# Kernel tuning notes

Measured on AMD Instinct MI355X. Metric: run time of the kernel, lower is better.

Reference implementation:

```python
import jax, jax.numpy as jnp
import numpy as np
import math

SEQ, BATCH, H, E, V = 2048, 64, 512, 256, 50257


def _gru_cell(x, h, W_ih, W_hh, b_ih, b_hh):
    # PyTorch GRU cell: gates ordered (r, z, n)
    gi = x @ W_ih.T + b_ih            # [B, 3H]
    gh = h @ W_hh.T + b_hh            # [B, 3H]
    i_r, i_z, i_n = jnp.split(gi, 3, axis=1)
    h_r, h_z, h_n = jnp.split(gh, 3, axis=1)
    r = jax.nn.sigmoid(i_r + h_r)
    z = jax.nn.sigmoid(i_z + h_z)
    n = jnp.tanh(i_n + r * h_n)
    return (1.0 - z) * n + z * h


def setup_inputs() -> dict:
    key = jax.random.key(0)
    ks = jax.random.split(key, 14)
    s = 1.0 / math.sqrt(H)
    inp = {
        "inputs": jax.random.randint(ks[0], (BATCH,), 0, V),
        "dec_hidden": jax.random.normal(ks[1], (2, BATCH, H), jnp.float32),
        "enc_outputs": jax.random.normal(ks[2], (SEQ, BATCH, H), jnp.float32),
        "emb": jax.random.normal(ks[3], (V, E), jnp.float32),
        # layer 0: input dim = H + E
        "W_ih0": jax.random.uniform(ks[4], (3 * H, H + E), jnp.float32, -s, s),
        "W_hh0": jax.random.uniform(ks[5], (3 * H, H), jnp.float32, -s, s),
        "b_ih0": jax.random.uniform(ks[6], (3 * H,), jnp.float32, -s, s),
        "b_hh0": jax.random.uniform(ks[7], (3 * H,), jnp.float32, -s, s),
        # layer 1: input dim = H
        "W_ih1": jax.random.uniform(ks[8], (3 * H, H), jnp.float32, -s, s),
        "W_hh1": jax.random.uniform(ks[9], (3 * H, H), jnp.float32, -s, s),
        "b_ih1": jax.random.uniform(ks[10], (3 * H,), jnp.float32, -s, s),
        "b_hh1": jax.random.uniform(ks[11], (3 * H,), jnp.float32, -s, s),
        "out_W": jax.random.uniform(ks[12], (V, H), jnp.float32, -s, s),
        "out_b": jax.random.uniform(ks[13], (V,), jnp.float32, -s, s),
    }
    return inp


def reference(inputs, dec_hidden, enc_outputs, emb,
              W_ih0, W_hh0, b_ih0, b_hh0,
              W_ih1, W_hh1, b_ih1, b_hh1,
              out_W, out_b):
    # --- dot-product attention (vectorized over seq) ---
    h_top = dec_hidden[-1]                                     # [B, H]
    scale = 1.0 / math.sqrt(H)
    energy = jnp.einsum('bh,sbh->sb', h_top, enc_outputs) * scale  # [S, B]
    alpha = jax.nn.softmax(energy, axis=0)                     # softmax over seq
    context = jnp.einsum('sb,sbh->bh', alpha, enc_outputs)     # [B, H]
    # --- embed + concat ---
    embeddings = emb[inputs]                                   # [B, E]
    x = jnp.concatenate([embeddings, context], axis=1)         # [B, E+H]
    # --- 2-layer GRU, single time step (eval mode: no dropout) ---
    h0 = _gru_cell(x, dec_hidden[0], W_ih0, W_hh0, b_ih0, b_hh0)
    h1 = _gru_cell(h0, dec_hidden[1], W_ih1, W_hh1, b_ih1, b_hh1)
    new_hidden = jnp.stack([h0, h1], axis=0)                   # [2, B, H]
    # --- vocab projection ---
    logits = h1 @ out_W.T + out_b                              # [B, V]
    return logits, new_hidden
```

## Files before the change

### kernel.cpp

```cpp
#include <hip/hip_runtime.h>
#include <math.h>

#define SEQ   2048
#define BATCH 64
#define HDIM  512
#define EDIM  256
#define VOCAB 50257
#define BH    (BATCH * HDIM)
#define G3    (3 * HDIM)
#define NCOL  (2 * G3)
#define P32   32
#define KS    4

typedef __attribute__((ext_vector_type(4))) float f32x4;
typedef __attribute__((ext_vector_type(8))) short bf16x8;

__device__ __forceinline__ unsigned short f2bf(float x) {
    unsigned int u = __float_as_uint(x);
    u += 0x7fffu + ((u >> 16) & 1u);
    return (unsigned short)(u >> 16);
}

__device__ __forceinline__ bf16x8 pack8(float4 a, float4 b) {
    bf16x8 r;
    r[0] = (short)f2bf(a.x); r[1] = (short)f2bf(a.y);
    r[2] = (short)f2bf(a.z); r[3] = (short)f2bf(a.w);
    r[4] = (short)f2bf(b.x); r[5] = (short)f2bf(b.y);
    r[6] = (short)f2bf(b.z); r[7] = (short)f2bf(b.w);
    return r;
}

__device__ __forceinline__ bf16x8 cvt8(const float* p) {
    return pack8(*(const float4*)p, *(const float4*)(p + 4));
}

__global__ __launch_bounds__(256)
void attn_partial(const float* __restrict__ enc, const float* __restrict__ dec,
                  float* __restrict__ pm, float* __restrict__ pl,
                  float* __restrict__ pacc) {
    const int lane = threadIdx.x & 63;
    const int w = threadIdx.x >> 6;
    const int p = blockIdx.x;
    const int b = blockIdx.y;
    const int s0 = (p * 4 + w) * 16;
    const float scale = 0.044194173824159216f;

    const float4* qp = (const float4*)(dec + BH + (size_t)b * HDIM + 8 * lane);
    float4 q0 = qp[0], q1 = qp[1];
    float qa[8] = {q0.x, q0.y, q0.z, q0.w, q1.x, q1.y, q1.z, q1.w};

    float m = -INFINITY, l = 0.f;
    float acc[8] = {0.f, 0.f, 0.f, 0.f, 0.f, 0.f, 0.f, 0.f};

    #pragma unroll 2
    for (int r = 0; r < 16; r += 4) {
        float va[4][8];
        #pragma unroll
        for (int j = 0; j < 4; ++j) {
            const float4* vp = (const float4*)(enc +
                ((size_t)(s0 + r + j) * BATCH + b) * HDIM + 8 * lane);
            float4 t0 = vp[0], t1 = vp[1];
            va[j][0] = t0.x; va[j][1] = t0.y; va[j][2] = t0.z; va[j][3] = t0.w;
            va[j][4] = t1.x; va[j][5] = t1.y; va[j][6] = t1.z; va[j][7] = t1.w;
        }
        float e[4];
        #pragma unroll
        for (int j = 0; j < 4; ++j) {
            float d = 0.f;
            #pragma unroll
            for (int i = 0; i < 8; ++i) d = fmaf(va[j][i], qa[i], d);
            e[j] = d;
        }
        #pragma unroll
        for (int off = 32; off > 0; off >>= 1) {
            #pragma unroll
            for (int j = 0; j < 4; ++j) e[j] += __shfl_xor(e[j], off, 64);
        }
        #pragma unroll
        for (int j = 0; j < 4; ++j) e[j] *= scale;
        float m4 = fmaxf(fmaxf(e[0], e[1]), fmaxf(e[2], e[3]));
        float em = fmaxf(m, m4);
        float f  = __expf(m - em);
        float w0 = __expf(e[0] - em), w1 = __expf(e[1] - em);
        float w2 = __expf(e[2] - em), w3 = __expf(e[3] - em);
        l = l * f + (w0 + w1 + w2 + w3);
        #pragma unroll
        for (int i = 0; i < 8; ++i) {
            float a = acc[i] * f;
            a = fmaf(w0, va[0][i], a);
            a = fmaf(w1, va[1][i], a);
            a = fmaf(w2, va[2][i], a);
            acc[i] = fmaf(w3, va[3][i], a);
        }
        m = em;
    }

    __shared__ float sacc[4][HDIM];
    __shared__ float sml[8];
    #pragma unroll
    for (int i = 0; i < 8; ++i) sacc[w][8 * lane + i] = acc[i];
    if (lane == 0) { sml[w] = m; sml[4 + w] = l; }
    __syncthreads();

    const float m0 = sml[0], m1 = sml[1], m2 = sml[2], m3 = sml[3];
    const float ms = fmaxf(fmaxf(m0, m1), fmaxf(m2, m3));
    const float c0 = __expf(m0 - ms), c1 = __expf(m1 - ms);
    const float c2 = __expf(m2 - ms), c3 = __expf(m3 - ms);
    const int t = threadIdx.x;
    #pragma unroll
    for (int i = 0; i < 2; ++i) {
        const int h = t + i * 256;
        float v = c0 * sacc[0][h] + c1 * sacc[1][h]
                + c2 * sacc[2][h] + c3 * sacc[3][h];
        pacc[((size_t)b * P32 + p) * HDIM + h] = v;
    }
    if (t == 0) {
        pm[b * P32 + p] = ms;
        pl[b * P32 + p] = c0 * sml[4] + c1 * sml[5] + c2 * sml[6] + c3 * sml[7];
    }
}

__global__ __launch_bounds__(512)
void attn_combine(const float* __restrict__ pm, const float* __restrict__ pl,
                  const float* __restrict__ pacc, const float* __restrict__ dec,
                  const float* __restrict__ emb, const int* __restrict__ inputs,
                  unsigned short* __restrict__ xbf,
                  unsigned short* __restrict__ d0bf,
                  unsigned short* __restrict__ d1bf) {
    __shared__ float s_coef[P32];
    __shared__ float s_inv;
    const int b = blockIdx.x;
    const int t = threadIdx.x;

    if (t < 64) {
        float mloc = -INFINITY;
        for (int p = t; p < P32; p += 64) mloc = fmaxf(mloc, pm[b * P32 + p]);
        #pragma unroll
        for (int off = 32; off > 0; off >>= 1) mloc = fmaxf(mloc, __shfl_xor(mloc, off, 64));
        float d = 0.f;
        for (int p = t; p < P32; p += 64) {
            float c = __expf(pm[b * P32 + p] - mloc);
            s_coef[p] = c;
            d = fmaf(c, pl[b * P32 + p], d);
        }
        #pragma unroll
        for (int off = 32; off > 0; off >>= 1) d += __shfl_xor(d, off, 64);
        if (t == 0) s_inv = 1.f / d;
    }
    __syncthreads();

    float c = 0.f;
    const float* pa = pacc + (size_t)b * P32 * HDIM + t;
    #pragma unroll 8
    for (int p = 0; p < P32; ++p) c = fmaf(s_coef[p], pa[(size_t)p * HDIM], c);
    float ctx = c * s_inv;

    xbf[(size_t)b * (EDIM + HDIM) + EDIM + t] = f2bf(ctx);
    if (t < EDIM)
        xbf[(size_t)b * (EDIM + HDIM) + t] = f2bf(emb[(size_t)inputs[b] * EDIM + t]);
    d0bf[(size_t)b * HDIM + t] = f2bf(dec[(size_t)b * HDIM + t]);
    d1bf[(size_t)b * HDIM + t] = f2bf(dec[BH + (size_t)b * HDIM + t]);
}

template<int K1>
__global__ __launch_bounds__(256)
void gru_gemm(const unsigned short* __restrict__ Aih,
              const unsigned short* __restrict__ Ahh,
              const float* __restrict__ Wih,
              const float* __restrict__ Whh,
              float* __restrict__ part) {
    const int lane = threadIdx.x & 63;
    const int nt = blockIdx.x * 4 + (threadIdx.x >> 6);
    const int kc = blockIdx.y;
    const int nn = lane & 15;
    const int koff = (lane >> 4) * 8;

    const bool ih = nt < 96;
    const int col16 = ih ? nt : nt - 96;
    const int g = col16 * 16 + nn;
    const int K = ih ? K1 : HDIM;
    const int kchunk = K >> 2;
    const int k0 = kc * kchunk;

    const float* wrow = (ih ? Wih : Whh) + (size_t)g * K + k0 + koff;
    const unsigned short* arow = (ih ? Aih : Ahh) + (size_t)nn * K + k0 + koff;

    f32x4 acc[4];
    #pragma unroll
    for (int mt = 0; mt < 4; ++mt) acc[mt] = (f32x4){0, 0, 0, 0};

    const int nks = kchunk >> 5;
    #pragma unroll 2
    for (int ks = 0; ks < nks; ++ks) {
        bf16x8 bf = cvt8(wrow + 32 * ks);
        #pragma unroll
        for (int mt = 0; mt < 4; ++mt) {
            bf16x8 a = *(const bf16x8*)(arow + (size_t)mt * 16 * K + 32 * ks);
            acc[mt] = __builtin_amdgcn_mfma_f32_16x16x32_bf16(a, bf, acc[mt], 0, 0, 0);
        }
    }

    const int col = col16 * 16 + nn + (ih ? 0 : G3);
    float* pp = part + ((size_t)kc * NCOL + col) * 64 + (lane >> 4) * 4;
    #pragma unroll
    for (int mt = 0; mt < 4; ++mt)
        *(f32x4*)(pp + mt * 16) = acc[mt];
}

__global__ __launch_bounds__(256)
void gru_gate(const float* __restrict__ part,
              const float* __restrict__ hprev,
              const float* __restrict__ bih, const float* __restrict__ bhh,
              float* __restrict__ hout, unsigned short* __restrict__ houtBf) {
    const int gidx = blockIdx.x * 256 + threadIdx.x;
    const int b = gidx & 63;
    const int h = gidx >> 6;

    #define PRD(c) (part[(size_t)(c) * 64 + b] \
                  + part[((size_t)NCOL + (c)) * 64 + b] \
                  + part[((size_t)2 * NCOL + (c)) * 64 + b] \
                  + part[((size_t)3 * NCOL + (c)) * 64 + b])
    float ir = PRD(h),             hr = PRD(G3 + h);
    float iz = PRD(HDIM + h),      hz = PRD(G3 + HDIM + h);
    float in_ = PRD(2 * HDIM + h), hn = PRD(G3 + 2 * HDIM + h);
    #undef PRD

    float r = 1.f / (1.f + __expf(-(ir + bih[h] + hr + bhh[h])));
    float z = 1.f / (1.f + __expf(-(iz + bih[HDIM + h] + hz + bhh[HDIM + h])));
    float n = tanhf(in_ + bih[2 * HDIM + h] + r * (hn + bhh[2 * HDIM + h]));
    float hp = hprev[(size_t)b * HDIM + h];
    float hnew = (1.f - z) * n + z * hp;

    hout[(size_t)b * HDIM + h] = hnew;
    houtBf[(size_t)b * HDIM + h] = f2bf(hnew);
}

__global__ __launch_bounds__(256)
void vocab_proj_mfma(const unsigned short* __restrict__ h1bf,
                     const float* __restrict__ Wout,
                     const float* __restrict__ bout,
                     float* __restrict__ logits) {
    __shared__ uint4 sh4[4096];
    const int t = threadIdx.x;
    const uint4* g4 = (const uint4*)h1bf;
    #pragma unroll
    for (int i = 0; i < 16; ++i) {
        int q = i * 256 + t;
        int r = q >> 6, s = q & 63;
        sh4[(r << 6) | (s ^ (r & 15))] = g4[q];
    }
    __syncthreads();

    const int NT = (VOCAB + 15) / 16;
    const int lane = t & 63;
    const int nt = blockIdx.x * 4 + (t >> 6);
    if (nt >= NT) return;

    const int nn = lane & 15;
    const int koff16 = lane >> 4;
    const int v  = nt * 16 + nn;
    const int vclamp = min(v, VOCAB - 1);

    const float* wrow = Wout + (size_t)vclamp * HDIM + koff16 * 8;

    f32x4 acc[4];
    #pragma unroll
    for (int mt = 0; mt < 4; ++mt) acc[mt] = (f32x4){0, 0, 0, 0};

    float4 pw0[3], pw1[3];
    #pragma unroll
    for (int d = 0; d < 3; ++d) {
        pw0[d] = *(const float4*)(wrow + 32 * d);
        pw1[d] = *(const float4*)(wrow + 32 * d + 4);
    }

    #pragma unroll
    for (int ks = 0; ks < 16; ++ks) {
        const int slot = ks % 3;
        bf16x8 bfrag = pack8(pw0[slot], pw1[slot]);
        if (ks + 3 < 16) {
            pw0[slot] = *(const float4*)(wrow + 32 * (ks + 3));
            pw1[slot] = *(const float4*)(wrow + 32 * (ks + 3) + 4);
        }
        const int s = 4 * ks + koff16;
        #pragma unroll
        for (int mt = 0; mt < 4; ++mt) {
            const int row = mt * 16 + nn;
            bf16x8 a = *(const bf16x8*)&sh4[(row << 6) | (s ^ nn)];
            acc[mt] = __builtin_amdgcn_mfma_f32_16x16x32_bf16(a, bfrag, acc[mt], 0, 0, 0);
        }
    }

    if (v < VOCAB) {
        const float bias = bout[v];
        const int b0 = koff16 * 4;
        #pragma unroll
        for (int mt = 0; mt < 4; ++mt)
            #pragma unroll
            for (int r = 0; r < 4; ++r)
                logits[(size_t)(mt * 16 + b0 + r) * VOCAB + v] = acc[mt][r] + bias;
    }
}

extern "C" void kernel_launch(void* const* d_in, const int* in_sizes, int n_in,
                              void* d_out, int out_size, void* d_ws, size_t ws_size,
                              hipStream_t stream) {
    const int*   inputs = (const int*)d_in[0];
    const float* dec    = (const float*)d_in[1];
    const float* enc    = (const float*)d_in[2];
    const float* emb    = (const float*)d_in[3];
    const float* Wih0   = (const float*)d_in[4];
    const float* Whh0   = (const float*)d_in[5];
    const float* bih0   = (const float*)d_in[6];
    const float* bhh0   = (const float*)d_in[7];
    const float* Wih1   = (const float*)d_in[8];
    const float* Whh1   = (const float*)d_in[9];
    const float* bih1   = (const float*)d_in[10];
    const float* bhh1   = (const float*)d_in[11];
    const float* Wout   = (const float*)d_in[12];
    const float* bout   = (const float*)d_in[13];
    float* out = (float*)d_out;

    float* w    = (float*)d_ws;
    float* pm   = w;
    float* pl   = pm + (size_t)P32 * BATCH;
    float* pacc = pl + (size_t)P32 * BATCH;
    float* part = pacc + (size_t)P32 * BATCH * HDIM;
    unsigned short* xbf  = (unsigned short*)(part + (size_t)KS * NCOL * 64);
    unsigned short* d0bf = xbf + (size_t)BATCH * (EDIM + HDIM);
    unsigned short* d1bf = d0bf + BH;
    unsigned short* h0bf = d1bf + BH;
    unsigned short* h1bf = h0bf + BH;

    float* h0out = out + (size_t)BATCH * VOCAB;
    float* h1out = h0out + BH;

    attn_partial<<<dim3(P32, BATCH), 256, 0, stream>>>(enc, dec, pm, pl, pacc);
    attn_combine<<<BATCH, 512, 0, stream>>>(pm, pl, pacc, dec, emb, inputs, xbf, d0bf, d1bf);

    gru_gemm<EDIM + HDIM><<<dim3(48, KS), 256, 0, stream>>>(xbf, d0bf, Wih0, Whh0, part);
    gru_gate<<<128, 256, 0, stream>>>(part, dec, bih0, bhh0, h0out, h0bf);
    gru_gemm<HDIM><<<dim3(48, KS), 256, 0, stream>>>(h0bf, d1bf, Wih1, Whh1, part);
    gru_gate<<<128, 256, 0, stream>>>(part, dec + BH, bih1, bhh1, h1out, h1bf);

    const int NT = (VOCAB + 15) / 16;
    vocab_proj_mfma<<<(NT + 3) / 4, 256, 0, stream>>>(h1bf, Wout, bout, out);
}
```

Measured before the change: 119.0 us.

## Fuse attention combine and both GRU layers into one persistent kernel with grid barriers

Replaces five separate launches (attention combine, two GRU GEMMs, two gate kernels) with a single 192-block kernel whose phases are separated by atomic-counter grid barriers. The aim is to remove per-launch overhead and inter-kernel gaps on this small, latency-bound middle section. In exchange it adds a memset of the barrier counters, spin-wait barriers whose correctness depends on all 192 blocks being co-resident, and a combine step in which every thread redundantly recomputes the softmax max and coefficients.

```diff
diff --git a/kernel.cpp b/kernel.cpp
--- a/kernel.cpp
+++ b/kernel.cpp
@@ -11,6 +11,7 @@
 #define NCOL  (2 * G3)
 #define P32   32
 #define KS    4
+#define NBLK_MID 192
 
 typedef __attribute__((ext_vector_type(4))) float f32x4;
 typedef __attribute__((ext_vector_type(8))) short bf16x8;
@@ -32,6 +33,16 @@
 
 __device__ __forceinline__ bf16x8 cvt8(const float* p) {
     return pack8(*(const float4*)p, *(const float4*)(p + 4));
+}
+
+__device__ __forceinline__ void gbar(unsigned* cnt, unsigned nb) {
+    __syncthreads();
+    if (threadIdx.x == 0) {
+        __hip_atomic_fetch_add(cnt, 1u, __ATOMIC_ACQ_REL, __HIP_MEMORY_SCOPE_AGENT);
+        while (__hip_atomic_load(cnt, __ATOMIC_ACQUIRE, __HIP_MEMORY_SCOPE_AGENT) < nb)
+            __builtin_amdgcn_s_sleep(2);
+    }
+    __syncthreads();
 }
 
 __global__ __launch_bounds__(256)
@@ -120,58 +131,15 @@
     }
 }
 
-__global__ __launch_bounds__(512)
-void attn_combine(const float* __restrict__ pm, const float* __restrict__ pl,
-                  const float* __restrict__ pacc, const float* __restrict__ dec,
-                  const float* __restrict__ emb, const int* __restrict__ inputs,
-                  unsigned short* __restrict__ xbf,
-                  unsigned short* __restrict__ d0bf,
-                  unsigned short* __restrict__ d1bf) {
-    __shared__ float s_coef[P32];
-    __shared__ float s_inv;
-    const int b = blockIdx.x;
-    const int t = threadIdx.x;
-
-    if (t < 64) {
-        float mloc = -INFINITY;
-        for (int p = t; p < P32; p += 64) mloc = fmaxf(mloc, pm[b * P32 + p]);
-        #pragma unroll
-        for (int off = 32; off > 0; off >>= 1) mloc = fmaxf(mloc, __shfl_xor(mloc, off, 64));
-        float d = 0.f;
-        for (int p = t; p < P32; p += 64) {
-            float c = __expf(pm[b * P32 + p] - mloc);
-            s_coef[p] = c;
-            d = fmaf(c, pl[b * P32 + p], d);
-        }
-        #pragma unroll
-        for (int off = 32; off > 0; off >>= 1) d += __shfl_xor(d, off, 64);
-        if (t == 0) s_inv = 1.f / d;
-    }
-    __syncthreads();
-
-    float c = 0.f;
-    const float* pa = pacc + (size_t)b * P32 * HDIM + t;
-    #pragma unroll 8
-    for (int p = 0; p < P32; ++p) c = fmaf(s_coef[p], pa[(size_t)p * HDIM], c);
-    float ctx = c * s_inv;
-
-    xbf[(size_t)b * (EDIM + HDIM) + EDIM + t] = f2bf(ctx);
-    if (t < EDIM)
-        xbf[(size_t)b * (EDIM + HDIM) + t] = f2bf(emb[(size_t)inputs[b] * EDIM + t]);
-    d0bf[(size_t)b * HDIM + t] = f2bf(dec[(size_t)b * HDIM + t]);
-    d1bf[(size_t)b * HDIM + t] = f2bf(dec[BH + (size_t)b * HDIM + t]);
-}
-
 template<int K1>
-__global__ __launch_bounds__(256)
-void gru_gemm(const unsigned short* __restrict__ Aih,
-              const unsigned short* __restrict__ Ahh,
-              const float* __restrict__ Wih,
-              const float* __restrict__ Whh,
-              float* __restrict__ part) {
-    const int lane = threadIdx.x & 63;
-    const int nt = blockIdx.x * 4 + (threadIdx.x >> 6);
-    const int kc = blockIdx.y;
+__device__ __forceinline__ void gemm_phase(int blk, int tid,
+        const unsigned short* __restrict__ Aih,
+        const unsigned short* __restrict__ Ahh,
+        const float* __restrict__ Wih, const float* __restrict__ Whh,
+        float* __restrict__ part) {
+    const int lane = tid & 63;
+    const int nt = (blk % 48) * 4 + (tid >> 6);
+    const int kc = blk / 48;
     const int nn = lane & 15;
     const int koff = (lane >> 4) * 8;
 
@@ -207,15 +175,12 @@
         *(f32x4*)(pp + mt * 16) = acc[mt];
 }
 
-__global__ __launch_bounds__(256)
-void gru_gate(const float* __restrict__ part,
-              const float* __restrict__ hprev,
-              const float* __restrict__ bih, const float* __restrict__ bhh,
-              float* __restrict__ hout, unsigned short* __restrict__ houtBf) {
-    const int gidx = blockIdx.x * 256 + threadIdx.x;
-    const int b = gidx & 63;
-    const int h = gidx >> 6;
-
+__device__ __forceinline__ void gate_phase(int idx,
+        const float* __restrict__ part, const float* __restrict__ hprev,
+        const float* __restrict__ bih, const float* __restrict__ bhh,
+        float* __restrict__ hout, unsigned short* __restrict__ houtBf) {
+    const int b = idx & 63;
+    const int h = idx >> 6;
     #define PRD(c) (part[(size_t)(c) * 64 + b] \
                   + part[((size_t)NCOL + (c)) * 64 + b] \
                   + part[((size_t)2 * NCOL + (c)) * 64 + b] \
@@ -224,15 +189,66 @@
     float iz = PRD(HDIM + h),      hz = PRD(G3 + HDIM + h);
     float in_ = PRD(2 * HDIM + h), hn = PRD(G3 + 2 * HDIM + h);
     #undef PRD
-
     float r = 1.f / (1.f + __expf(-(ir + bih[h] + hr + bhh[h])));
     float z = 1.f / (1.f + __expf(-(iz + bih[HDIM + h] + hz + bhh[HDIM + h])));
     float n = tanhf(in_ + bih[2 * HDIM + h] + r * (hn + bhh[2 * HDIM + h]));
     float hp = hprev[(size_t)b * HDIM + h];
     float hnew = (1.f - z) * n + z * hp;
-
     hout[(size_t)b * HDIM + h] = hnew;
     houtBf[(size_t)b * HDIM + h] = f2bf(hnew);
+}
+
+__global__ __launch_bounds__(256)
+void mid_fused(unsigned* __restrict__ bars,
+               const float* __restrict__ pm, const float* __restrict__ pl,
+               const float* __restrict__ pacc, const float* __restrict__ dec,
+               const float* __restrict__ emb, const int* __restrict__ inputs,
+               const float* __restrict__ Wih0, const float* __restrict__ Whh0,
+               const float* __restrict__ bih0, const float* __restrict__ bhh0,
+               const float* __restrict__ Wih1, const float* __restrict__ Whh1,
+               const float* __restrict__ bih1, const float* __restrict__ bhh1,
+               unsigned short* __restrict__ xbf, unsigned short* __restrict__ d0bf,
+               unsigned short* __restrict__ d1bf, float* __restrict__ part,
+               float* __restrict__ h0out, unsigned short* __restrict__ h0bf,
+               float* __restrict__ h1out, unsigned short* __restrict__ h1bf) {
+    const int blk = blockIdx.x;
+    const int tid = threadIdx.x;
+    const int idx = blk * 256 + tid;
+
+    if (idx < BH) {
+        const int b = idx >> 9, h = idx & 511;
+        float mmax = -INFINITY;
+        #pragma unroll 8
+        for (int p = 0; p < P32; ++p) mmax = fmaxf(mmax, pm[b * P32 + p]);
+        float denom = 0.f, ctx = 0.f;
+        const float* pa = pacc + (size_t)b * P32 * HDIM + h;
+        #pragma unroll 4
+        for (int p = 0; p < P32; ++p) {
+            float c = __expf(pm[b * P32 + p] - mmax);
+            denom = fmaf(c, pl[b * P32 + p], denom);
+            ctx = fmaf(c, pa[(size_t)p * HDIM], ctx);
+        }
+        ctx *= (1.f / denom);
+        xbf[(size_t)b * (EDIM + HDIM) + EDIM + h] = f2bf(ctx);
+        d0bf[idx] = f2bf(dec[idx]);
+        d1bf[idx] = f2bf(dec[BH + idx]);
+    } else {
+        const int j = idx - BH;
+        const int b = j >> 8, e = j & 255;
+        xbf[(size_t)b * (EDIM + HDIM) + e] = f2bf(emb[(size_t)inputs[b] * EDIM + e]);
+    }
+    gbar(bars + 0, NBLK_MID);
+
+    gemm_phase<EDIM + HDIM>(blk, tid, xbf, d0bf, Wih0, Whh0, part);
+    gbar(bars + 1, NBLK_MID);
+
+    if (idx < BH) gate_phase(idx, part, dec, bih0, bhh0, h0out, h0bf);
+    gbar(bars + 2, NBLK_MID);
+
+    gemm_phase<HDIM>(blk, tid, h0bf, d1bf, Wih1, Whh1, part);
+    gbar(bars + 3, NBLK_MID);
+
+    if (idx < BH) gate_phase(idx, part, dec + BH, bih1, bhh1, h1out, h1bf);
 }
 
 __global__ __launch_bounds__(256)
@@ -321,7 +337,8 @@
     const float* bout   = (const float*)d_in[13];
     float* out = (float*)d_out;
 
-    float* w    = (float*)d_ws;
+    unsigned* bars = (unsigned*)d_ws;
+    float* w    = (float*)((char*)d_ws + 64);
     float* pm   = w;
     float* pl   = pm + (size_t)P32 * BATCH;
     float* pacc = pl + (size_t)P32 * BATCH;
@@ -335,13 +352,15 @@
     float* h0out = out + (size_t)BATCH * VOCAB;
     float* h1out = h0out + BH;
 
+    hipMemsetAsync(bars, 0, 64, stream);
+
     attn_partial<<<dim3(P32, BATCH), 256, 0, stream>>>(enc, dec, pm, pl, pacc);
-    attn_combine<<<BATCH, 512, 0, stream>>>(pm, pl, pacc, dec, emb, inputs, xbf, d0bf, d1bf);
-
-    gru_gemm<EDIM + HDIM><<<dim3(48, KS), 256, 0, stream>>>(xbf, d0bf, Wih0, Whh0, part);
-    gru_gate<<<128, 256, 0, stream>>>(part, dec, bih0, bhh0, h0out, h0bf);
-    gru_gemm<HDIM><<<dim3(48, KS), 256, 0, stream>>>(h0bf, d1bf, Wih1, Whh1, part);
-    gru_gate<<<128, 256, 0, stream>>>(part, dec + BH, bih1, bhh1, h1out, h1bf);
+
+    mid_fused<<<NBLK_MID, 256, 0, stream>>>(bars, pm, pl, pacc, dec, emb, inputs,
+                                            Wih0, Whh0, bih0, bhh0,
+                                            Wih1, Whh1, bih1, bhh1,
+                                            xbf, d0bf, d1bf, part,
+                                            h0out, h0bf, h1out, h1bf);
 
     const int NT = (VOCAB + 15) / 16;
     vocab_proj_mfma<<<(NT + 3) / 4, 256, 0, stream>>>(h1bf, Wout, bout, out);
```

Result: slower. 179.4 us (+50.7%).

## Fuse attention combine into partial kernel via last-block atomic ticket

Applied to the files above, without the earlier changes.

Removes the separate attn_combine launch: each attention partial block increments a per-batch atomic ticket, and the last of the 32 blocks for that batch row merges the partial softmax states and writes the bf16 context, embedding and hidden copies. Encoder loads also switch to nontemporal loads so the streamed data does not pollute the cache. This saves one kernel launch and its gap, at the cost of a serialized tail block per batch row. The ticket is never reset but relies on modulo 32 across calls, and the pacc reads in the last block depend on acquire/release ordering being sufficient.

```diff
diff --git a/kernel.cpp b/kernel.cpp
--- a/kernel.cpp
+++ b/kernel.cpp
@@ -36,8 +36,19 @@
 
 __global__ __launch_bounds__(256)
 void attn_partial(const float* __restrict__ enc, const float* __restrict__ dec,
+                  const float* __restrict__ emb, const int* __restrict__ inputs,
+                  unsigned* __restrict__ ticket,
                   float* __restrict__ pm, float* __restrict__ pl,
-                  float* __restrict__ pacc) {
+                  float* __restrict__ pacc,
+                  unsigned short* __restrict__ xbf,
+                  unsigned short* __restrict__ d0bf,
+                  unsigned short* __restrict__ d1bf) {
+    __shared__ float sacc[4][HDIM];
+    __shared__ float sml[8];
+    __shared__ unsigned s_old;
+    __shared__ float cs[P32];
+    __shared__ float s_inv;
+
     const int lane = threadIdx.x & 63;
     const int w = threadIdx.x >> 6;
     const int p = blockIdx.x;
@@ -57,11 +68,12 @@
         float va[4][8];
         #pragma unroll
         for (int j = 0; j < 4; ++j) {
-            const float4* vp = (const float4*)(enc +
+            const f32x4* vp = (const f32x4*)(enc +
                 ((size_t)(s0 + r + j) * BATCH + b) * HDIM + 8 * lane);
-            float4 t0 = vp[0], t1 = vp[1];
-            va[j][0] = t0.x; va[j][1] = t0.y; va[j][2] = t0.z; va[j][3] = t0.w;
-            va[j][4] = t1.x; va[j][5] = t1.y; va[j][6] = t1.z; va[j][7] = t1.w;
+            f32x4 t0 = __builtin_nontemporal_load(vp);
+            f32x4 t1 = __builtin_nontemporal_load(vp + 1);
+            #pragma unroll
+            for (int i = 0; i < 4; ++i) { va[j][i] = t0[i]; va[j][4 + i] = t1[i]; }
         }
         float e[4];
         #pragma unroll
@@ -95,8 +107,6 @@
         m = em;
     }
 
-    __shared__ float sacc[4][HDIM];
-    __shared__ float sml[8];
     #pragma unroll
     for (int i = 0; i < 8; ++i) sacc[w][8 * lane + i] = acc[i];
     if (lane == 0) { sml[w] = m; sml[4 + w] = l; }
@@ -118,48 +128,42 @@
         pm[b * P32 + p] = ms;
         pl[b * P32 + p] = c0 * sml[4] + c1 * sml[5] + c2 * sml[6] + c3 * sml[7];
     }
-}
-
-__global__ __launch_bounds__(512)
-void attn_combine(const float* __restrict__ pm, const float* __restrict__ pl,
-                  const float* __restrict__ pacc, const float* __restrict__ dec,
-                  const float* __restrict__ emb, const int* __restrict__ inputs,
-                  unsigned short* __restrict__ xbf,
-                  unsigned short* __restrict__ d0bf,
-                  unsigned short* __restrict__ d1bf) {
-    __shared__ float s_coef[P32];
-    __shared__ float s_inv;
-    const int b = blockIdx.x;
-    const int t = threadIdx.x;
-
-    if (t < 64) {
-        float mloc = -INFINITY;
-        for (int p = t; p < P32; p += 64) mloc = fmaxf(mloc, pm[b * P32 + p]);
-        #pragma unroll
-        for (int off = 32; off > 0; off >>= 1) mloc = fmaxf(mloc, __shfl_xor(mloc, off, 64));
-        float d = 0.f;
-        for (int p = t; p < P32; p += 64) {
-            float c = __expf(pm[b * P32 + p] - mloc);
-            s_coef[p] = c;
-            d = fmaf(c, pl[b * P32 + p], d);
-        }
-        #pragma unroll
-        for (int off = 32; off > 0; off >>= 1) d += __shfl_xor(d, off, 64);
+    __syncthreads();
+
+    if (t == 0)
+        s_old = __hip_atomic_fetch_add(&ticket[b], 1u, __ATOMIC_ACQ_REL,
+                                       __HIP_MEMORY_SCOPE_AGENT);
+    __syncthreads();
+    if ((s_old & 31u) != 31u) return;
+
+    if (t < 32) {
+        float pmv = pm[b * P32 + t];
+        float mm = pmv;
+        #pragma unroll
+        for (int off = 16; off > 0; off >>= 1) mm = fmaxf(mm, __shfl_xor(mm, off, 64));
+        float c = __expf(pmv - mm);
+        cs[t] = c;
+        float d = c * pl[b * P32 + t];
+        #pragma unroll
+        for (int off = 16; off > 0; off >>= 1) d += __shfl_xor(d, off, 64);
         if (t == 0) s_inv = 1.f / d;
     }
     __syncthreads();
 
-    float c = 0.f;
-    const float* pa = pacc + (size_t)b * P32 * HDIM + t;
-    #pragma unroll 8
-    for (int p = 0; p < P32; ++p) c = fmaf(s_coef[p], pa[(size_t)p * HDIM], c);
-    float ctx = c * s_inv;
-
-    xbf[(size_t)b * (EDIM + HDIM) + EDIM + t] = f2bf(ctx);
+    const float* pa = pacc + (size_t)b * P32 * HDIM;
+    #pragma unroll
+    for (int i = 0; i < 2; ++i) {
+        const int h = t + i * 256;
+        float c = 0.f;
+        #pragma unroll 8
+        for (int pp = 0; pp < P32; ++pp)
+            c = fmaf(cs[pp], pa[(size_t)pp * HDIM + h], c);
+        xbf[(size_t)b * (EDIM + HDIM) + EDIM + h] = f2bf(c * s_inv);
+        d0bf[(size_t)b * HDIM + h] = f2bf(dec[(size_t)b * HDIM + h]);
+        d1bf[(size_t)b * HDIM + h] = f2bf(dec[BH + (size_t)b * HDIM + h]);
+    }
     if (t < EDIM)
         xbf[(size_t)b * (EDIM + HDIM) + t] = f2bf(emb[(size_t)inputs[b] * EDIM + t]);
-    d0bf[(size_t)b * HDIM + t] = f2bf(dec[(size_t)b * HDIM + t]);
-    d1bf[(size_t)b * HDIM + t] = f2bf(dec[BH + (size_t)b * HDIM + t]);
 }
 
 template<int K1>
@@ -321,7 +325,8 @@
     const float* bout   = (const float*)d_in[13];
     float* out = (float*)d_out;
 
-    float* w    = (float*)d_ws;
+    unsigned* ticket = (unsigned*)d_ws;
+    float* w    = (float*)((char*)d_ws + 256);
     float* pm   = w;
     float* pl   = pm + (size_t)P32 * BATCH;
     float* pacc = pl + (size_t)P32 * BATCH;
@@ -335,8 +340,9 @@
     float* h0out = out + (size_t)BATCH * VOCAB;
     float* h1out = h0out + BH;
 
-    attn_partial<<<dim3(P32, BATCH), 256, 0, stream>>>(enc, dec, pm, pl, pacc);
-    attn_combine<<<BATCH, 512, 0, stream>>>(pm, pl, pacc, dec, emb, inputs, xbf, d0bf, d1bf);
+    attn_partial<<<dim3(P32, BATCH), 256, 0, stream>>>(enc, dec, emb, inputs,
+                                                       ticket, pm, pl, pacc,
+                                                       xbf, d0bf, d1bf);
 
     gru_gemm<EDIM + HDIM><<<dim3(48, KS), 256, 0, stream>>>(xbf, d0bf, Wih0, Whh0, part);
     gru_gate<<<128, 256, 0, stream>>>(part, dec, bih0, bhh0, h0out, h0bf);
```

After: 209.6 us. 1.76x slower.
